# Performance work log

Measured on AMD Instinct MI355X. Metric: run time of the kernel, lower is better.

Reference implementation:

```python
import jax, jax.numpy as jnp
import numpy as np

N_NODES = 50000
N_EDGES = 400000
N_FEAT = 128
HIDDEN = 128
N_HEADS = 4
HEADC = HIDDEN // N_HEADS  # 32
N_CLASSES = 10
K_HOPS = 3
CST = 1e-5


def setup_inputs() -> dict:
    key = jax.random.key(0)
    ks = jax.random.split(key, 12)
    s = 1.0 / np.sqrt(HIDDEN)
    return {
        "node_feat": jax.random.normal(ks[0], (N_NODES, N_FEAT), jnp.float32),
        "edge_index": jax.random.randint(ks[1], (2, N_EDGES), 0, N_NODES, jnp.int64),
        # Linear weights stored as [in, out] so forward is x @ W + b
        "Wt": jax.random.normal(ks[2], (N_FEAT, HIDDEN), jnp.float32) / np.sqrt(N_FEAT),
        "bt": jax.random.normal(ks[3], (HIDDEN,), jnp.float32) * 0.01,
        "Wq": jax.random.normal(ks[4], (HIDDEN, N_HEADS * HEADC), jnp.float32) * s,
        "bq": jax.random.normal(ks[5], (N_HEADS * HEADC,), jnp.float32) * 0.01,
        "Wk": jax.random.normal(ks[6], (HIDDEN, N_HEADS * HEADC), jnp.float32) * s,
        "bk": jax.random.normal(ks[7], (N_HEADS * HEADC,), jnp.float32) * 0.01,
        "Wv": jax.random.normal(ks[8], (HIDDEN, N_HEADS * N_CLASSES), jnp.float32) * s,
        "bv": jax.random.normal(ks[9], (N_HEADS * N_CLASSES,), jnp.float32) * 0.01,
        "hopwise": jnp.ones((K_HOPS + 1,), jnp.float32),          # Parameter(ones(K+1))
        "headwise": jax.random.normal(ks[10], (N_HEADS, K_HOPS), jnp.float32) * 0.1,  # Parameter, zeros at init; randomized for testing
    }


def reference(node_feat, edge_index, Wt, bt, Wq, bq, Wk, bk, Wv, bv, hopwise, headwise):
    N = node_feat.shape[0]
    row, col = edge_index[0], edge_index[1]

    # eval mode: dropout is identity
    x = jax.nn.relu(node_feat @ Wt + bt)                       # [N, hidden]
    Q = (1.0 + jax.nn.elu(x @ Wq + bq)).reshape(N, N_HEADS, HEADC)
    Kf = (1.0 + jax.nn.elu(x @ Wk + bk)).reshape(N, N_HEADS, HEADC)
    V = (x @ Wv + bv).reshape(N, N_HEADS, N_CLASSES)

    M = jnp.einsum('nhi,nhj->nhij', Kf, V)                     # [N, H, headc, C]
    hidden = V * hopwise[0]                                     # ind_gamma & gamma_softmax branch
    layerwise = jax.nn.softmax(headwise, axis=0)                # softmax over heads (dim=-2)

    for hop in range(K_HOPS):
        # PyG sum aggregation, source_to_target: out[col] += x[row]
        M = jax.ops.segment_sum(M[row], col, num_segments=N)
        Kf = jax.ops.segment_sum(Kf[row], col, num_segments=N)
        H = jnp.einsum('nhi,nhij->nhj', Q, M)                  # [N, H, C]
        C = jnp.einsum('nhi,nhi->nh', Q, Kf)[..., None] + CST  # [N, H, 1]
        H = H / C
        gamma = hopwise[hop + 1] * layerwise[:, hop][:, None]  # [H, 1]
        hidden = hidden + gamma * H

    return hidden.sum(axis=-2)                                  # multi_concat=False: sum over heads -> [N, C]
```

## Files before the change

kernel.cpp:

```cpp
#include <hip/hip_runtime.h>
#include <hip/hip_bf16.h>

#define NN 50000
#define NE 400000
#define NF 128
#define HID 128
#define NH 4
#define HC 32
#define NC 10
#define KHOPS 3
#define NBLK ((NN + 1023) / 1024)

typedef unsigned int uint;
typedef unsigned short ushort;
typedef __attribute__((ext_vector_type(8))) short bf16x8;
typedef __attribute__((ext_vector_type(4))) float f32x4;
typedef __attribute__((ext_vector_type(2))) float f32x2;

__global__ void detect_kernel(const int* __restrict__ ei, int* __restrict__ flag) {
    int w = ei[2 * threadIdx.x + 1];
    unsigned long long b = __ballot(w != 0);
    if (threadIdx.x == 0) *flag = (b == 0ULL) ? 1 : 0;
}

__device__ __forceinline__ int edge_row(const int* ei, int is64, int e) {
    return is64 ? ei[2 * e] : ei[e];
}
__device__ __forceinline__ int edge_col(const int* ei, int is64, int e) {
    return is64 ? ei[2 * NE + 2 * e] : ei[NE + e];
}

__global__ void zero_kernel(int* __restrict__ p, int n) {
    int i = blockIdx.x * blockDim.x + threadIdx.x;
    if (i < n) p[i] = 0;
}

__global__ void hist_kernel(const int* __restrict__ ei, const int* __restrict__ flag,
                            int* __restrict__ counts) {
    int e = blockIdx.x * blockDim.x + threadIdx.x;
    if (e >= NE) return;
    int c = edge_col(ei, *flag, e);
    atomicAdd(&counts[c], 1);
}

__global__ __launch_bounds__(256) void bsum_kernel(const int* __restrict__ counts,
                                                   int* __restrict__ bsum) {
    int b = blockIdx.x, tid = threadIdx.x;
    int base = b * 1024 + tid * 4;
    int4 v = {0, 0, 0, 0};
    if (base < NN) v = *(const int4*)(counts + base);
    int s = v.x + v.y + v.z + v.w;
#pragma unroll
    for (int off = 32; off >= 1; off >>= 1) s += __shfl_xor(s, off);
    __shared__ int ws[4];
    int lane = tid & 63, w = tid >> 6;
    if (lane == 0) ws[w] = s;
    __syncthreads();
    if (tid == 0) bsum[b] = ws[0] + ws[1] + ws[2] + ws[3];
}

__global__ void bscan_kernel(const int* __restrict__ bsum, int* __restrict__ boff,
                             int* __restrict__ rowptr) {
    int lane = threadIdx.x;
    int v = (lane < NBLK) ? bsum[lane] : 0;
    int t = v;
#pragma unroll
    for (int off = 1; off < 64; off <<= 1) {
        int u = __shfl_up(t, off);
        if (lane >= off) t += u;
    }
    if (lane < NBLK) boff[lane] = t - v;
    if (lane == NBLK - 1) rowptr[NN] = t;
}

__global__ __launch_bounds__(256) void scanb_kernel(const int* __restrict__ counts,
                                                    const int* __restrict__ boff,
                                                    int* __restrict__ rowptr,
                                                    int* __restrict__ cursor) {
    int b = blockIdx.x, tid = threadIdx.x;
    int base = b * 1024 + tid * 4;
    int4 v = {0, 0, 0, 0};
    if (base < NN) v = *(const int4*)(counts + base);
    int s3 = v.x + v.y + v.z + v.w;
    int lane = tid & 63, w = tid >> 6;
    int t = s3;
#pragma unroll
    for (int off = 1; off < 64; off <<= 1) {
        int u = __shfl_up(t, off);
        if (lane >= off) t += u;
    }
    __shared__ int ws[4];
    if (lane == 63) ws[w] = t;
    __syncthreads();
    int wofs = boff[b];
    for (int i = 0; i < 4; i++) wofs += (i < w) ? ws[i] : 0;
    int excl = wofs + t - s3;
    if (base < NN) {
        int4 o;
        o.x = excl;
        o.y = excl + v.x;
        o.z = o.y + v.y;
        o.w = o.z + v.z;
        *(int4*)(rowptr + base) = o;
        *(int4*)(cursor + base) = o;
    }
}

__global__ void scatter_kernel(const int* __restrict__ ei, const int* __restrict__ flag,
                               int* __restrict__ cursor, int* __restrict__ srows) {
    int e = blockIdx.x * blockDim.x + threadIdx.x;
    if (e >= NE) return;
    int is64 = *flag;
    int r = edge_row(ei, is64, e);
    int c = edge_col(ei, is64, e);
    int pos = atomicAdd(&cursor[c], 1);
    srows[pos] = r;
}

__device__ __forceinline__ short bfbits(float f) {
    __hip_bfloat16 h = __float2bfloat16(f);
    return *reinterpret_cast<short*>(&h);
}
__device__ __forceinline__ ushort bfbitsu(float f) {
    __hip_bfloat16 h = __float2bfloat16(f);
    return *reinterpret_cast<ushort*>(&h);
}
__device__ __forceinline__ float bflo(uint u) { return __uint_as_float(u << 16); }
__device__ __forceinline__ float bfhi(uint u) { return __uint_as_float(u & 0xFFFF0000u); }
__device__ __forceinline__ float bfs(ushort u) { return __uint_as_float(((uint)u) << 16); }

template<bool HI>
__device__ __forceinline__ uint pk8(float a, float b, uint old) {
    return __builtin_amdgcn_cvt_pk_fp8_f32(a, b, old, HI);
}
template<bool HI>
__device__ __forceinline__ f32x2 upk8(uint w) {
    return __builtin_amdgcn_cvt_pk_f32_fp8(w, HI);
}

__global__ void wconv_kernel(const float* __restrict__ Wt, const float* __restrict__ Wq,
                             const float* __restrict__ Wk, const float* __restrict__ Wv,
                             ushort* __restrict__ Wtb, ushort* __restrict__ Wqkvb) {
    int idx = blockIdx.x * 256 + threadIdx.x;
    if (idx < 128 * 128) {
        int c = idx >> 7, k = idx & 127;
        Wtb[c * 128 + k] = bfbitsu(Wt[k * 128 + c]);
    }
    if (idx < 304 * 128) {
        int c = idx >> 7, k = idx & 127;
        float w;
        if (c < 128) w = Wq[k * 128 + c];
        else if (c < 256) w = Wk[k * 128 + (c - 128)];
        else { int cv = c - 256; w = (cv < 40) ? Wv[k * 40 + cv] : 0.f; }
        Wqkvb[c * 128 + k] = bfbitsu(w);
    }
}

__global__ __launch_bounds__(256) void xm_kernel(const float* __restrict__ nf,
                                                 const ushort* __restrict__ Wtb,
                                                 const float* __restrict__ bt,
                                                 ushort* __restrict__ xb) {
    int wid = threadIdx.x >> 6, lane = threadIdx.x & 63;
    int row0 = blockIdx.x * 64 + wid * 16;
    int r = lane & 15, kg = lane >> 4;
    int ar = row0 + r;
    if (ar > NN - 1) ar = NN - 1;
    int ctbeg = blockIdx.y * 4;
    f32x4 acc[4];
#pragma unroll
    for (int ct = 0; ct < 4; ct++) acc[ct] = f32x4{0.f, 0.f, 0.f, 0.f};
#pragma unroll
    for (int ks = 0; ks < 4; ks++) {
        int k0 = ks * 32 + kg * 8;
        const float4* ap = (const float4*)(nf + (size_t)ar * 128 + k0);
        float4 a0 = ap[0], a1 = ap[1];
        bf16x8 af;
        af[0] = bfbits(a0.x); af[1] = bfbits(a0.y); af[2] = bfbits(a0.z); af[3] = bfbits(a0.w);
        af[4] = bfbits(a1.x); af[5] = bfbits(a1.y); af[6] = bfbits(a1.z); af[7] = bfbits(a1.w);
#pragma unroll
        for (int ct = 0; ct < 4; ct++) {
            bf16x8 bfr = *(const bf16x8*)(Wtb + (size_t)((ctbeg + ct) * 16 + r) * 128 + k0);
            acc[ct] = __builtin_amdgcn_mfma_f32_16x16x32_bf16(af, bfr, acc[ct], 0, 0, 0);
        }
    }
#pragma unroll
    for (int ct = 0; ct < 4; ct++) {
        int c = (ctbeg + ct) * 16 + r;
        float b = bt[c];
#pragma unroll
        for (int reg = 0; reg < 4; reg++) {
            int n = row0 + kg * 4 + reg;
            if (n < NN) {
                float z = acc[ct][reg] + b;
                xb[(size_t)n * 128 + c] = bfbitsu(fmaxf(z, 0.f));
            }
        }
    }
}

template<int CTBEG, int NCT>
__device__ __forceinline__ void qkv_body(const ushort* __restrict__ xb,
                                         const ushort* __restrict__ Wqkvb,
                                         const float* __restrict__ bq,
                                         const float* __restrict__ bk,
                                         const float* __restrict__ bv,
                                         float* __restrict__ Qp,
                                         ushort* __restrict__ Kpp,
                                         ushort* __restrict__ Vbf,
                                         int row0, int r, int kg) {
    int ar = row0 + r;
    if (ar > NN - 1) ar = NN - 1;
    f32x4 acc[NCT];
#pragma unroll
    for (int ct = 0; ct < NCT; ct++) acc[ct] = f32x4{0.f, 0.f, 0.f, 0.f};
#pragma unroll
    for (int ks = 0; ks < 4; ks++) {
        int k0 = ks * 32 + kg * 8;
        bf16x8 af = *(const bf16x8*)(xb + (size_t)ar * 128 + k0);
#pragma unroll
        for (int ct = 0; ct < NCT; ct++) {
            bf16x8 bfr = *(const bf16x8*)(Wqkvb + (size_t)((CTBEG + ct) * 16 + r) * 128 + k0);
            acc[ct] = __builtin_amdgcn_mfma_f32_16x16x32_bf16(af, bfr, acc[ct], 0, 0, 0);
        }
    }
#pragma unroll
    for (int ct = 0; ct < NCT; ct++) {
        int c = (CTBEG + ct) * 16 + r;
        float bias;
        if (c < 128) bias = bq[c];
        else if (c < 256) bias = bk[c - 128];
        else { int cv = c - 256; bias = (cv < 40) ? bv[cv] : 0.f; }
#pragma unroll
        for (int reg = 0; reg < 4; reg++) {
            int n = row0 + kg * 4 + reg;
            if (n >= NN) continue;
            float z = acc[ct][reg] + bias;
            if (c < 128) {
                float q = z > 0.f ? 1.f + z : __expf(z);
                Qp[(size_t)n * 128 + c] = q;
            } else if (c < 256) {
                int cc = c - 128;
                float kv = z > 0.f ? 1.f + z : __expf(z);
                Kpp[(size_t)n * 128 + cc] = bfbitsu(kv);
            } else {
                int cv = c - 256;
                if (cv < 40) {
                    int hh = cv / 10, cc = cv - hh * 10;
                    Vbf[(size_t)n * 64 + hh * 16 + cc] = bfbitsu(z);
                }
            }
        }
    }
}

__global__ __launch_bounds__(256) void qkv_kernel(const ushort* __restrict__ xb,
                                                  const ushort* __restrict__ Wqkvb,
                                                  const float* __restrict__ bq,
                                                  const float* __restrict__ bk,
                                                  const float* __restrict__ bv,
                                                  float* __restrict__ Qp,
                                                  ushort* __restrict__ Kpp,
                                                  ushort* __restrict__ Vbf) {
    int wid = threadIdx.x >> 6, lane = threadIdx.x & 63;
    int row0 = blockIdx.x * 64 + wid * 16;
    int r = lane & 15, kg = lane >> 4;
    if (blockIdx.y == 0)
        qkv_body<0, 8>(xb, Wqkvb, bq, bk, bv, Qp, Kpp, Vbf, row0, r, kg);
    else if (blockIdx.y == 1)
        qkv_body<8, 8>(xb, Wqkvb, bq, bk, bv, Qp, Kpp, Vbf, row0, r, kg);
    else
        qkv_body<16, 3>(xb, Wqkvb, bq, bk, bv, Qp, Kpp, Vbf, row0, r, kg);
}

__global__ void vinit_kernel(float* __restrict__ out, const ushort* __restrict__ Vbf,
                             const float* __restrict__ hopwise) {
    int idx = blockIdx.x * blockDim.x + threadIdx.x;
    if (idx >= NN * NC) return;
    int n = idx / NC, c = idx - n * NC;
    const ushort* v = Vbf + (size_t)n * 64 + c;
    out[idx] = hopwise[0] * (bfs(v[0]) + bfs(v[16]) + bfs(v[32]) + bfs(v[48]));
}

__device__ __forceinline__ void fused_epilog(float a0[10], float a1[10], float k0a, float k1a,
                                             int gw, int lane,
                                             const float* __restrict__ Qp,
                                             float* __restrict__ out,
                                             uint4* __restrict__ Mq4n, uint* __restrict__ Mrun,
                                             ushort* __restrict__ Kn,
                                             const float* __restrict__ hopwise,
                                             const float* __restrict__ headwise,
                                             int hop, int write_next,
                                             float h_scale, float ss) {
    int p0 = lane * 2;
    float2 q = *(const float2*)(Qp + (size_t)gw * 128 + p0);
    float num[10];
#pragma unroll
    for (int c = 0; c < 10; c++) num[c] = q.x * a0[c] + q.y * a1[c];
    float den = q.x * k0a + q.y * k1a;
#pragma unroll
    for (int off = 8; off >= 1; off >>= 1) {
#pragma unroll
        for (int c = 0; c < 10; c++) num[c] += __shfl_xor(num[c], off);
        den += __shfl_xor(den, off);
    }
    float e0 = __expf(headwise[0 * KHOPS + hop]);
    float e1 = __expf(headwise[1 * KHOPS + hop]);
    float e2 = __expf(headwise[2 * KHOPS + hop]);
    float e3 = __expf(headwise[3 * KHOPS + hop]);
    int h = lane >> 4;
    float eh = (h == 0) ? e0 : (h == 1) ? e1 : (h == 2) ? e2 : e3;
    float gamma = hopwise[hop + 1] * eh / (e0 + e1 + e2 + e3);
    float s = h_scale * gamma / (den + 1e-5f);
    float tot[10];
#pragma unroll
    for (int c = 0; c < 10; c++) {
        tot[c] = s * num[c];
        tot[c] += __shfl_xor(tot[c], 16);
        tot[c] += __shfl_xor(tot[c], 32);
    }
    if (lane < 10) {
        float v = lane == 0 ? tot[0] : lane == 1 ? tot[1] : lane == 2 ? tot[2] :
                  lane == 3 ? tot[3] : lane == 4 ? tot[4] : lane == 5 ? tot[5] :
                  lane == 6 ? tot[6] : lane == 7 ? tot[7] : lane == 8 ? tot[8] : tot[9];
        out[(size_t)gw * 10 + lane] += v;
    }
    if (write_next) {
        uint4 o;
        uint x = pk8<false>(a0[0] * ss, a0[1] * ss, 0u);
        o.x = pk8<true>(a0[2] * ss, a0[3] * ss, x);
        x = pk8<false>(a0[4] * ss, a0[5] * ss, 0u);
        o.y = pk8<true>(a0[6] * ss, a0[7] * ss, x);
        x = pk8<false>(a1[0] * ss, a1[1] * ss, 0u);
        o.z = pk8<true>(a1[2] * ss, a1[3] * ss, x);
        x = pk8<false>(a1[4] * ss, a1[5] * ss, 0u);
        o.w = pk8<true>(a1[6] * ss, a1[7] * ss, x);
        Mq4n[(size_t)gw * 64 + lane] = o;
        x = pk8<false>(a0[8] * ss, a0[9] * ss, 0u);
        x = pk8<true>(a1[8] * ss, a1[9] * ss, x);
        Mrun[(size_t)gw * 64 + lane] = x;
        uint kw = (uint)bfbitsu(k0a) | (((uint)bfbitsu(k1a)) << 16);
        *(uint*)(Kn + (size_t)gw * 128 + p0) = kw;
    }
}

__device__ __forceinline__ void edge_acc(float a0[10], float a1[10], float& k0a, float& k1a,
                                         uint4 mq, uint mr, uint kk) {
    f32x2 f;
    f = upk8<false>(mq.x); a0[0] += f.x; a0[1] += f.y;
    f = upk8<true>(mq.x);  a0[2] += f.x; a0[3] += f.y;
    f = upk8<false>(mq.y); a0[4] += f.x; a0[5] += f.y;
    f = upk8<true>(mq.y);  a0[6] += f.x; a0[7] += f.y;
    f = upk8<false>(mq.z); a1[0] += f.x; a1[1] += f.y;
    f = upk8<true>(mq.z);  a1[2] += f.x; a1[3] += f.y;
    f = upk8<false>(mq.w); a1[4] += f.x; a1[5] += f.y;
    f = upk8<true>(mq.w);  a1[6] += f.x; a1[7] += f.y;
    f = upk8<false>(mr);   a0[8] += f.x; a0[9] += f.y;
    f = upk8<true>(mr);    a1[8] += f.x; a1[9] += f.y;
    k0a += bflo(kk);
    k1a += bfhi(kk);
}

__global__ __launch_bounds__(256) void aggf0_kernel(const ushort* __restrict__ Kpp,
                                                    const ushort* __restrict__ Vbf,
                                                    const float* __restrict__ Qp,
                                                    float* __restrict__ out,
                                                    uint4* __restrict__ Mq4n, uint* __restrict__ Mrun,
                                                    ushort* __restrict__ Kn,
                                                    const int* __restrict__ rowptr,
                                                    const int* __restrict__ srows,
                                                    const float* __restrict__ hopwise,
                                                    const float* __restrict__ headwise) {
    int gw = (blockIdx.x * 256 + threadIdx.x) >> 6;
    int lane = threadIdx.x & 63;
    int p0 = lane * 2;
    int h = lane >> 4;
    int beg = rowptr[gw], end = rowptr[gw + 1];
    float a0[10] = {0.f}, a1[10] = {0.f};
    float k0a = 0.f, k1a = 0.f;
    int e = beg;
    for (; e + 1 < end; e += 2) {
        int s0 = srows[e], s1 = srows[e + 1];
        uint kk0 = *(const uint*)(Kpp + (size_t)s0 * 128 + p0);
        uint kk1 = *(const uint*)(Kpp + (size_t)s1 * 128 + p0);
        const ushort* vb0 = Vbf + (size_t)s0 * 64 + h * 16;
        const ushort* vb1 = Vbf + (size_t)s1 * 64 + h * 16;
        uint4 v40 = *(const uint4*)vb0; uint v10 = *(const uint*)(vb0 + 8);
        uint4 v41 = *(const uint4*)vb1; uint v11 = *(const uint*)(vb1 + 8);
        float k00 = bflo(kk0), k01 = bfhi(kk0);
        float k10 = bflo(kk1), k11 = bfhi(kk1);
        k0a += k00 + k10; k1a += k01 + k11;
        float vv0[10] = {bflo(v40.x), bfhi(v40.x), bflo(v40.y), bfhi(v40.y), bflo(v40.z),
                         bfhi(v40.z), bflo(v40.w), bfhi(v40.w), bflo(v10), bfhi(v10)};
        float vv1[10] = {bflo(v41.x), bfhi(v41.x), bflo(v41.y), bfhi(v41.y), bflo(v41.z),
                         bfhi(v41.z), bflo(v41.w), bfhi(v41.w), bflo(v11), bfhi(v11)};
#pragma unroll
        for (int c = 0; c < 10; c++) {
            a0[c] += k00 * vv0[c] + k10 * vv1[c];
            a1[c] += k01 * vv0[c] + k11 * vv1[c];
        }
    }
    for (; e < end; ++e) {
        int s0 = srows[e];
        uint kk0 = *(const uint*)(Kpp + (size_t)s0 * 128 + p0);
        const ushort* vb0 = Vbf + (size_t)s0 * 64 + h * 16;
        uint4 v40 = *(const uint4*)vb0; uint v10 = *(const uint*)(vb0 + 8);
        float k00 = bflo(kk0), k01 = bfhi(kk0);
        k0a += k00; k1a += k01;
        float vv0[10] = {bflo(v40.x), bfhi(v40.x), bflo(v40.y), bfhi(v40.y), bflo(v40.z),
                         bfhi(v40.z), bflo(v40.w), bfhi(v40.w), bflo(v10), bfhi(v10)};
#pragma unroll
        for (int c = 0; c < 10; c++) {
            a0[c] += k00 * vv0[c];
            a1[c] += k01 * vv0[c];
        }
    }
    fused_epilog(a0, a1, k0a, k1a, gw, lane, Qp, out, Mq4n, Mrun, Kn,
                 hopwise, headwise, 0, 1, 1.0f, 0.0625f);
}

__global__ __launch_bounds__(256) void aggf_kernel(const uint4* __restrict__ Mq4,
                                                   const uint* __restrict__ Mru,
                                                   const ushort* __restrict__ Kc,
                                                   const float* __restrict__ Qp,
                                                   float* __restrict__ out,
                                                   uint4* __restrict__ Mq4n, uint* __restrict__ Mrun,
                                                   ushort* __restrict__ Kn,
                                                   const int* __restrict__ rowptr,
                                                   const int* __restrict__ srows,
                                                   const float* __restrict__ hopwise,
                                                   const float* __restrict__ headwise,
                                                   int hop, int write_next) {
    int gw = (blockIdx.x * 256 + threadIdx.x) >> 6;
    int lane = threadIdx.x & 63;
    const uint* Kcu = (const uint*)Kc;
    int beg = rowptr[gw], end = rowptr[gw + 1];
    float a0[10] = {0.f}, a1[10] = {0.f};
    float k0a = 0.f, k1a = 0.f;
    int e = beg;
    for (; e + 3 < end; e += 4) {
        int s0 = srows[e], s1 = srows[e + 1], s2 = srows[e + 2], s3 = srows[e + 3];
        uint4 m0 = Mq4[(size_t)s0 * 64 + lane];
        uint4 m1 = Mq4[(size_t)s1 * 64 + lane];
        uint4 m2 = Mq4[(size_t)s2 * 64 + lane];
        uint4 m3 = Mq4[(size_t)s3 * 64 + lane];
        uint r0 = Mru[(size_t)s0 * 64 + lane];
        uint r1 = Mru[(size_t)s1 * 64 + lane];
        uint r2 = Mru[(size_t)s2 * 64 + lane];
        uint r3 = Mru[(size_t)s3 * 64 + lane];
        uint K0 = Kcu[(size_t)s0 * 64 + lane];
        uint K1 = Kcu[(size_t)s1 * 64 + lane];
        uint K2 = Kcu[(size_t)s2 * 64 + lane];
        uint K3 = Kcu[(size_t)s3 * 64 + lane];
        edge_acc(a0, a1, k0a, k1a, m0, r0, K0);
        edge_acc(a0, a1, k0a, k1a, m1, r1, K1);
        edge_acc(a0, a1, k0a, k1a, m2, r2, K2);
        edge_acc(a0, a1, k0a, k1a, m3, r3, K3);
    }
    for (; e < end; ++e) {
        int s0 = srows[e];
        uint4 m0 = Mq4[(size_t)s0 * 64 + lane];
        uint r0 = Mru[(size_t)s0 * 64 + lane];
        uint K0 = Kcu[(size_t)s0 * 64 + lane];
        edge_acc(a0, a1, k0a, k1a, m0, r0, K0);
    }
    fused_epilog(a0, a1, k0a, k1a, gw, lane, Qp, out, Mq4n, Mrun, Kn,
                 hopwise, headwise, hop, write_next, 16.0f, 1.0f);
}

extern "C" void kernel_launch(void* const* d_in, const int* in_sizes, int n_in,
                              void* d_out, int out_size, void* d_ws, size_t ws_size,
                              hipStream_t stream) {
    const float* nf = (const float*)d_in[0];
    const int* ei = (const int*)d_in[1];
    const float* Wt = (const float*)d_in[2];
    const float* bt = (const float*)d_in[3];
    const float* Wq = (const float*)d_in[4];
    const float* bq = (const float*)d_in[5];
    const float* Wk = (const float*)d_in[6];
    const float* bk = (const float*)d_in[7];
    const float* Wv = (const float*)d_in[8];
    const float* bv = (const float*)d_in[9];
    const float* hopwise = (const float*)d_in[10];
    const float* headwise = (const float*)d_in[11];
    float* out = (float*)d_out;

    char* p = (char*)d_ws;
    auto alloc = [&](size_t bytes) {
        char* r = p;
        p += (bytes + 255) & ~(size_t)255;
        return r;
    };
    int* rowptr = (int*)alloc((NN + 4) * sizeof(int));
    int* cursor = (int*)alloc((NN + 4) * sizeof(int));
    int* bsum = (int*)alloc(NBLK * sizeof(int));
    int* boff = (int*)alloc(NBLK * sizeof(int));
    int* srows = (int*)alloc((size_t)NE * sizeof(int));
    int* flag = (int*)alloc(sizeof(int));
    ushort* Wtb = (ushort*)alloc(128 * 128 * sizeof(ushort));
    ushort* Wqkvb = (ushort*)alloc(304 * 128 * sizeof(ushort));
    float* Qp = (float*)alloc((size_t)NN * 128 * sizeof(float));
    ushort* Kpp = (ushort*)alloc((size_t)NN * 128 * sizeof(ushort));
    ushort* Vbf = (ushort*)alloc((size_t)NN * 64 * sizeof(ushort));
    ushort* Ka = (ushort*)alloc((size_t)NN * 128 * sizeof(ushort));
    uint4* Mq4a = (uint4*)alloc((size_t)NN * 64 * sizeof(uint4));
    uint4* Mq4b = (uint4*)alloc((size_t)NN * 64 * sizeof(uint4));
    uint* Mrua = (uint*)alloc((size_t)NN * 64 * sizeof(uint));
    uint* Mrub = (uint*)alloc((size_t)NN * 64 * sizeof(uint));
    ushort* xb = (ushort*)Mq4a;
    ushort* Kb = Kpp;

    detect_kernel<<<1, 64, 0, stream>>>(ei, flag);
    zero_kernel<<<(NN + 255) / 256, 256, 0, stream>>>(cursor, NN);
    hist_kernel<<<(NE + 255) / 256, 256, 0, stream>>>(ei, flag, cursor);
    bsum_kernel<<<NBLK, 256, 0, stream>>>(cursor, bsum);
    bscan_kernel<<<1, 64, 0, stream>>>(bsum, boff, rowptr);
    scanb_kernel<<<NBLK, 256, 0, stream>>>(cursor, boff, rowptr, cursor);
    scatter_kernel<<<(NE + 255) / 256, 256, 0, stream>>>(ei, flag, cursor, srows);

    wconv_kernel<<<(304 * 128 + 255) / 256, 256, 0, stream>>>(Wt, Wq, Wk, Wv, Wtb, Wqkvb);
    int nrb = (NN + 63) / 64;
    xm_kernel<<<dim3(nrb, 2), 256, 0, stream>>>(nf, Wtb, bt, xb);
    qkv_kernel<<<dim3(nrb, 3), 256, 0, stream>>>(xb, Wqkvb, bq, bk, bv, Qp, Kpp, Vbf);
    vinit_kernel<<<(NN * NC + 255) / 256, 256, 0, stream>>>(out, Vbf, hopwise);

    aggf0_kernel<<<NN / 4, 256, 0, stream>>>(Kpp, Vbf, Qp, out, Mq4a, Mrua, Ka,
                                             rowptr, srows, hopwise, headwise);
    aggf_kernel<<<NN / 4, 256, 0, stream>>>(Mq4a, Mrua, Ka, Qp, out, Mq4b, Mrub, Kb,
                                            rowptr, srows, hopwise, headwise, 1, 1);
    aggf_kernel<<<NN / 4, 256, 0, stream>>>(Mq4b, Mrub, Kb, Qp, out, Mq4a, Mrua, Ka,
                                            rowptr, srows, hopwise, headwise, 2, 0);
}
```

Baseline: 391.1 us.

## Store K features in fp8 with 1/16 scale and use packed f32x2 accumulation

```diff
diff --git a/kernel.cpp b/kernel.cpp
--- a/kernel.cpp
+++ b/kernel.cpp
@@ -128,6 +128,9 @@
 __device__ __forceinline__ float bflo(uint u) { return __uint_as_float(u << 16); }
 __device__ __forceinline__ float bfhi(uint u) { return __uint_as_float(u & 0xFFFF0000u); }
 __device__ __forceinline__ float bfs(ushort u) { return __uint_as_float(((uint)u) << 16); }
+__device__ __forceinline__ f32x2 bf2(uint u) {
+    return f32x2{__uint_as_float(u << 16), __uint_as_float(u & 0xFFFF0000u)};
+}
 
 template<bool HI>
 __device__ __forceinline__ uint pk8(float a, float b, uint old) {
@@ -205,7 +208,7 @@
                                          const float* __restrict__ bk,
                                          const float* __restrict__ bv,
                                          float* __restrict__ Qp,
-                                         ushort* __restrict__ Kpp,
+                                         unsigned char* __restrict__ K8,
                                          ushort* __restrict__ Vbf,
                                          int row0, int r, int kg) {
     int ar = row0 + r;
@@ -240,8 +243,9 @@
                 Qp[(size_t)n * 128 + c] = q;
             } else if (c < 256) {
                 int cc = c - 128;
-                float kv = z > 0.f ? 1.f + z : __expf(z);
-                Kpp[(size_t)n * 128 + cc] = bfbitsu(kv);
+                float kv = (z > 0.f ? 1.f + z : __expf(z)) * 0.0625f;
+                uint w = pk8<false>(kv, 0.f, 0u);
+                K8[(size_t)n * 128 + cc] = (unsigned char)(w & 0xFF);
             } else {
                 int cv = c - 256;
                 if (cv < 40) {
@@ -259,17 +263,17 @@
                                                   const float* __restrict__ bk,
                                                   const float* __restrict__ bv,
                                                   float* __restrict__ Qp,
-                                                  ushort* __restrict__ Kpp,
+                                                  unsigned char* __restrict__ K8,
                                                   ushort* __restrict__ Vbf) {
     int wid = threadIdx.x >> 6, lane = threadIdx.x & 63;
     int row0 = blockIdx.x * 64 + wid * 16;
     int r = lane & 15, kg = lane >> 4;
     if (blockIdx.y == 0)
-        qkv_body<0, 8>(xb, Wqkvb, bq, bk, bv, Qp, Kpp, Vbf, row0, r, kg);
+        qkv_body<0, 8>(xb, Wqkvb, bq, bk, bv, Qp, K8, Vbf, row0, r, kg);
     else if (blockIdx.y == 1)
-        qkv_body<8, 8>(xb, Wqkvb, bq, bk, bv, Qp, Kpp, Vbf, row0, r, kg);
+        qkv_body<8, 8>(xb, Wqkvb, bq, bk, bv, Qp, K8, Vbf, row0, r, kg);
     else
-        qkv_body<16, 3>(xb, Wqkvb, bq, bk, bv, Qp, Kpp, Vbf, row0, r, kg);
+        qkv_body<16, 3>(xb, Wqkvb, bq, bk, bv, Qp, K8, Vbf, row0, r, kg);
 }
 
 __global__ void vinit_kernel(float* __restrict__ out, const ushort* __restrict__ Vbf,
@@ -281,22 +285,24 @@
     out[idx] = hopwise[0] * (bfs(v[0]) + bfs(v[16]) + bfs(v[32]) + bfs(v[48]));
 }
 
-__device__ __forceinline__ void fused_epilog(float a0[10], float a1[10], float k0a, float k1a,
+__device__ __forceinline__ void fused_epilog(f32x2 A0[5], f32x2 A1[5], f32x2 kA,
                                              int gw, int lane,
                                              const float* __restrict__ Qp,
                                              float* __restrict__ out,
                                              uint4* __restrict__ Mq4n, uint* __restrict__ Mrun,
-                                             ushort* __restrict__ Kn,
+                                             ushort* __restrict__ K8n,
                                              const float* __restrict__ hopwise,
                                              const float* __restrict__ headwise,
-                                             int hop, int write_next,
-                                             float h_scale, float ss) {
+                                             int hop, int write_next) {
     int p0 = lane * 2;
     float2 q = *(const float2*)(Qp + (size_t)gw * 128 + p0);
     float num[10];
 #pragma unroll
-    for (int c = 0; c < 10; c++) num[c] = q.x * a0[c] + q.y * a1[c];
-    float den = q.x * k0a + q.y * k1a;
+    for (int j = 0; j < 5; j++) {
+        num[2 * j] = q.x * A0[j].x + q.y * A1[j].x;
+        num[2 * j + 1] = q.x * A0[j].y + q.y * A1[j].y;
+    }
+    float den = q.x * kA.x + q.y * kA.y;
 #pragma unroll
     for (int off = 8; off >= 1; off >>= 1) {
 #pragma unroll
@@ -310,7 +316,7 @@
     int h = lane >> 4;
     float eh = (h == 0) ? e0 : (h == 1) ? e1 : (h == 2) ? e2 : e3;
     float gamma = hopwise[hop + 1] * eh / (e0 + e1 + e2 + e3);
-    float s = h_scale * gamma / (den + 1e-5f);
+    float s = gamma / (den + 6.25e-7f);
     float tot[10];
 #pragma unroll
     for (int c = 0; c < 10; c++) {
@@ -326,105 +332,98 @@
     }
     if (write_next) {
         uint4 o;
-        uint x = pk8<false>(a0[0] * ss, a0[1] * ss, 0u);
-        o.x = pk8<true>(a0[2] * ss, a0[3] * ss, x);
-        x = pk8<false>(a0[4] * ss, a0[5] * ss, 0u);
-        o.y = pk8<true>(a0[6] * ss, a0[7] * ss, x);
-        x = pk8<false>(a1[0] * ss, a1[1] * ss, 0u);
-        o.z = pk8<true>(a1[2] * ss, a1[3] * ss, x);
-        x = pk8<false>(a1[4] * ss, a1[5] * ss, 0u);
-        o.w = pk8<true>(a1[6] * ss, a1[7] * ss, x);
+        o.x = pk8<true>(A0[1].x, A0[1].y, pk8<false>(A0[0].x, A0[0].y, 0u));
+        o.y = pk8<true>(A0[3].x, A0[3].y, pk8<false>(A0[2].x, A0[2].y, 0u));
+        o.z = pk8<true>(A1[1].x, A1[1].y, pk8<false>(A1[0].x, A1[0].y, 0u));
+        o.w = pk8<true>(A1[3].x, A1[3].y, pk8<false>(A1[2].x, A1[2].y, 0u));
         Mq4n[(size_t)gw * 64 + lane] = o;
-        x = pk8<false>(a0[8] * ss, a0[9] * ss, 0u);
-        x = pk8<true>(a1[8] * ss, a1[9] * ss, x);
-        Mrun[(size_t)gw * 64 + lane] = x;
-        uint kw = (uint)bfbitsu(k0a) | (((uint)bfbitsu(k1a)) << 16);
-        *(uint*)(Kn + (size_t)gw * 128 + p0) = kw;
-    }
-}
-
-__device__ __forceinline__ void edge_acc(float a0[10], float a1[10], float& k0a, float& k1a,
+        Mrun[(size_t)gw * 64 + lane] =
+            pk8<true>(A1[4].x, A1[4].y, pk8<false>(A0[4].x, A0[4].y, 0u));
+        uint kw = pk8<false>(kA.x, kA.y, 0u);
+        K8n[(size_t)gw * 64 + lane] = (ushort)(kw & 0xFFFF);
+    }
+}
+
+__device__ __forceinline__ void edge_acc(f32x2 A0[5], f32x2 A1[5], f32x2& kA,
                                          uint4 mq, uint mr, uint kk) {
-    f32x2 f;
-    f = upk8<false>(mq.x); a0[0] += f.x; a0[1] += f.y;
-    f = upk8<true>(mq.x);  a0[2] += f.x; a0[3] += f.y;
-    f = upk8<false>(mq.y); a0[4] += f.x; a0[5] += f.y;
-    f = upk8<true>(mq.y);  a0[6] += f.x; a0[7] += f.y;
-    f = upk8<false>(mq.z); a1[0] += f.x; a1[1] += f.y;
-    f = upk8<true>(mq.z);  a1[2] += f.x; a1[3] += f.y;
-    f = upk8<false>(mq.w); a1[4] += f.x; a1[5] += f.y;
-    f = upk8<true>(mq.w);  a1[6] += f.x; a1[7] += f.y;
-    f = upk8<false>(mr);   a0[8] += f.x; a0[9] += f.y;
-    f = upk8<true>(mr);    a1[8] += f.x; a1[9] += f.y;
-    k0a += bflo(kk);
-    k1a += bfhi(kk);
-}
-
-__global__ __launch_bounds__(256) void aggf0_kernel(const ushort* __restrict__ Kpp,
+    A0[0] += upk8<false>(mq.x);
+    A0[1] += upk8<true>(mq.x);
+    A0[2] += upk8<false>(mq.y);
+    A0[3] += upk8<true>(mq.y);
+    A1[0] += upk8<false>(mq.z);
+    A1[1] += upk8<true>(mq.z);
+    A1[2] += upk8<false>(mq.w);
+    A1[3] += upk8<true>(mq.w);
+    A0[4] += upk8<false>(mr);
+    A1[4] += upk8<true>(mr);
+    kA += upk8<false>(kk);
+}
+
+__global__ __launch_bounds__(256) void aggf0_kernel(const ushort* __restrict__ K8c,
                                                     const ushort* __restrict__ Vbf,
                                                     const float* __restrict__ Qp,
                                                     float* __restrict__ out,
                                                     uint4* __restrict__ Mq4n, uint* __restrict__ Mrun,
-                                                    ushort* __restrict__ Kn,
+                                                    ushort* __restrict__ K8n,
                                                     const int* __restrict__ rowptr,
                                                     const int* __restrict__ srows,
                                                     const float* __restrict__ hopwise,
                                                     const float* __restrict__ headwise) {
     int gw = (blockIdx.x * 256 + threadIdx.x) >> 6;
     int lane = threadIdx.x & 63;
-    int p0 = lane * 2;
     int h = lane >> 4;
     int beg = rowptr[gw], end = rowptr[gw + 1];
-    float a0[10] = {0.f}, a1[10] = {0.f};
-    float k0a = 0.f, k1a = 0.f;
+    f32x2 A0[5], A1[5], kA = f32x2{0.f, 0.f};
+#pragma unroll
+    for (int j = 0; j < 5; j++) { A0[j] = f32x2{0.f, 0.f}; A1[j] = f32x2{0.f, 0.f}; }
     int e = beg;
     for (; e + 1 < end; e += 2) {
         int s0 = srows[e], s1 = srows[e + 1];
-        uint kk0 = *(const uint*)(Kpp + (size_t)s0 * 128 + p0);
-        uint kk1 = *(const uint*)(Kpp + (size_t)s1 * 128 + p0);
+        uint k0w = K8c[(size_t)s0 * 64 + lane];
+        uint k1w = K8c[(size_t)s1 * 64 + lane];
         const ushort* vb0 = Vbf + (size_t)s0 * 64 + h * 16;
         const ushort* vb1 = Vbf + (size_t)s1 * 64 + h * 16;
         uint4 v40 = *(const uint4*)vb0; uint v10 = *(const uint*)(vb0 + 8);
         uint4 v41 = *(const uint4*)vb1; uint v11 = *(const uint*)(vb1 + 8);
-        float k00 = bflo(kk0), k01 = bfhi(kk0);
-        float k10 = bflo(kk1), k11 = bfhi(kk1);
-        k0a += k00 + k10; k1a += k01 + k11;
-        float vv0[10] = {bflo(v40.x), bfhi(v40.x), bflo(v40.y), bfhi(v40.y), bflo(v40.z),
-                         bfhi(v40.z), bflo(v40.w), bfhi(v40.w), bflo(v10), bfhi(v10)};
-        float vv1[10] = {bflo(v41.x), bfhi(v41.x), bflo(v41.y), bfhi(v41.y), bflo(v41.z),
-                         bfhi(v41.z), bflo(v41.w), bfhi(v41.w), bflo(v11), bfhi(v11)};
-#pragma unroll
-        for (int c = 0; c < 10; c++) {
-            a0[c] += k00 * vv0[c] + k10 * vv1[c];
-            a1[c] += k01 * vv0[c] + k11 * vv1[c];
+        f32x2 kk0 = upk8<false>(k0w);
+        f32x2 kk1 = upk8<false>(k1w);
+        kA += kk0 + kk1;
+        f32x2 V0[5] = {bf2(v40.x), bf2(v40.y), bf2(v40.z), bf2(v40.w), bf2(v10)};
+        f32x2 V1[5] = {bf2(v41.x), bf2(v41.y), bf2(v41.z), bf2(v41.w), bf2(v11)};
+        f32x2 k00 = f32x2{kk0.x, kk0.x}, k01 = f32x2{kk0.y, kk0.y};
+        f32x2 k10 = f32x2{kk1.x, kk1.x}, k11 = f32x2{kk1.y, kk1.y};
+#pragma unroll
+        for (int j = 0; j < 5; j++) {
+            A0[j] += k00 * V0[j] + k10 * V1[j];
+            A1[j] += k01 * V0[j] + k11 * V1[j];
         }
     }
     for (; e < end; ++e) {
         int s0 = srows[e];
-        uint kk0 = *(const uint*)(Kpp + (size_t)s0 * 128 + p0);
+        uint k0w = K8c[(size_t)s0 * 64 + lane];
         const ushort* vb0 = Vbf + (size_t)s0 * 64 + h * 16;
         uint4 v40 = *(const uint4*)vb0; uint v10 = *(const uint*)(vb0 + 8);
-        float k00 = bflo(kk0), k01 = bfhi(kk0);
-        k0a += k00; k1a += k01;
-        float vv0[10] = {bflo(v40.x), bfhi(v40.x), bflo(v40.y), bfhi(v40.y), bflo(v40.z),
-                         bfhi(v40.z), bflo(v40.w), bfhi(v40.w), bflo(v10), bfhi(v10)};
-#pragma unroll
-        for (int c = 0; c < 10; c++) {
-            a0[c] += k00 * vv0[c];
-            a1[c] += k01 * vv0[c];
+        f32x2 kk0 = upk8<false>(k0w);
+        kA += kk0;
+        f32x2 V0[5] = {bf2(v40.x), bf2(v40.y), bf2(v40.z), bf2(v40.w), bf2(v10)};
+        f32x2 k00 = f32x2{kk0.x, kk0.x}, k01 = f32x2{kk0.y, kk0.y};
+#pragma unroll
+        for (int j = 0; j < 5; j++) {
+            A0[j] += k00 * V0[j];
+            A1[j] += k01 * V0[j];
         }
     }
-    fused_epilog(a0, a1, k0a, k1a, gw, lane, Qp, out, Mq4n, Mrun, Kn,
-                 hopwise, headwise, 0, 1, 1.0f, 0.0625f);
+    fused_epilog(A0, A1, kA, gw, lane, Qp, out, Mq4n, Mrun, K8n,
+                 hopwise, headwise, 0, 1);
 }
 
 __global__ __launch_bounds__(256) void aggf_kernel(const uint4* __restrict__ Mq4,
                                                    const uint* __restrict__ Mru,
-                                                   const ushort* __restrict__ Kc,
+                                                   const ushort* __restrict__ K8c,
                                                    const float* __restrict__ Qp,
                                                    float* __restrict__ out,
                                                    uint4* __restrict__ Mq4n, uint* __restrict__ Mrun,
-                                                   ushort* __restrict__ Kn,
+                                                   ushort* __restrict__ K8n,
                                                    const int* __restrict__ rowptr,
                                                    const int* __restrict__ srows,
                                                    const float* __restrict__ hopwise,
@@ -432,39 +431,48 @@
                                                    int hop, int write_next) {
     int gw = (blockIdx.x * 256 + threadIdx.x) >> 6;
     int lane = threadIdx.x & 63;
-    const uint* Kcu = (const uint*)Kc;
     int beg = rowptr[gw], end = rowptr[gw + 1];
-    float a0[10] = {0.f}, a1[10] = {0.f};
-    float k0a = 0.f, k1a = 0.f;
+    f32x2 A0[5], A1[5], kA = f32x2{0.f, 0.f};
+#pragma unroll
+    for (int j = 0; j < 5; j++) { A0[j] = f32x2{0.f, 0.f}; A1[j] = f32x2{0.f, 0.f}; }
     int e = beg;
-    for (; e + 3 < end; e += 4) {
-        int s0 = srows[e], s1 = srows[e + 1], s2 = srows[e + 2], s3 = srows[e + 3];
+    for (; e + 5 < end; e += 6) {
+        int s0 = srows[e], s1 = srows[e + 1], s2 = srows[e + 2];
+        int s3 = srows[e + 3], s4 = srows[e + 4], s5 = srows[e + 5];
         uint4 m0 = Mq4[(size_t)s0 * 64 + lane];
         uint4 m1 = Mq4[(size_t)s1 * 64 + lane];
         uint4 m2 = Mq4[(size_t)s2 * 64 + lane];
         uint4 m3 = Mq4[(size_t)s3 * 64 + lane];
+        uint4 m4 = Mq4[(size_t)s4 * 64 + lane];
+        uint4 m5 = Mq4[(size_t)s5 * 64 + lane];
         uint r0 = Mru[(size_t)s0 * 64 + lane];
         uint r1 = Mru[(size_t)s1 * 64 + lane];
         uint r2 = Mru[(size_t)s2 * 64 + lane];
         uint r3 = Mru[(size_t)s3 * 64 + lane];
-        uint K0 = Kcu[(size_t)s0 * 64 + lane];
-        uint K1 = Kcu[(size_t)s1 * 64 + lane];
-        uint K2 = Kcu[(size_t)s2 * 64 + lane];
-        uint K3 = Kcu[(size_t)s3 * 64 + lane];
-        edge_acc(a0, a1, k0a, k1a, m0, r0, K0);
-        edge_acc(a0, a1, k0a, k1a, m1, r1, K1);
-        edge_acc(a0, a1, k0a, k1a, m2, r2, K2);
-        edge_acc(a0, a1, k0a, k1a, m3, r3, K3);
+        uint r4 = Mru[(size_t)s4 * 64 + lane];
+        uint r5 = Mru[(size_t)s5 * 64 + lane];
+        uint k0 = K8c[(size_t)s0 * 64 + lane];
+        uint k1 = K8c[(size_t)s1 * 64 + lane];
+        uint k2 = K8c[(size_t)s2 * 64 + lane];
+        uint k3 = K8c[(size_t)s3 * 64 + lane];
+        uint k4 = K8c[(size_t)s4 * 64 + lane];
+        uint k5 = K8c[(size_t)s5 * 64 + lane];
+        edge_acc(A0, A1, kA, m0, r0, k0);
+        edge_acc(A0, A1, kA, m1, r1, k1);
+        edge_acc(A0, A1, kA, m2, r2, k2);
+        edge_acc(A0, A1, kA, m3, r3, k3);
+        edge_acc(A0, A1, kA, m4, r4, k4);
+        edge_acc(A0, A1, kA, m5, r5, k5);
     }
     for (; e < end; ++e) {
         int s0 = srows[e];
         uint4 m0 = Mq4[(size_t)s0 * 64 + lane];
         uint r0 = Mru[(size_t)s0 * 64 + lane];
-        uint K0 = Kcu[(size_t)s0 * 64 + lane];
-        edge_acc(a0, a1, k0a, k1a, m0, r0, K0);
-    }
-    fused_epilog(a0, a1, k0a, k1a, gw, lane, Qp, out, Mq4n, Mrun, Kn,
-                 hopwise, headwise, hop, write_next, 16.0f, 1.0f);
+        uint k0 = K8c[(size_t)s0 * 64 + lane];
+        edge_acc(A0, A1, kA, m0, r0, k0);
+    }
+    fused_epilog(A0, A1, kA, gw, lane, Qp, out, Mq4n, Mrun, K8n,
+                 hopwise, headwise, hop, write_next);
 }
 
 extern "C" void kernel_launch(void* const* d_in, const int* in_sizes, int n_in,
@@ -499,15 +507,15 @@
     ushort* Wtb = (ushort*)alloc(128 * 128 * sizeof(ushort));
     ushort* Wqkvb = (ushort*)alloc(304 * 128 * sizeof(ushort));
     float* Qp = (float*)alloc((size_t)NN * 128 * sizeof(float));
-    ushort* Kpp = (ushort*)alloc((size_t)NN * 128 * sizeof(ushort));
+    unsigned char* K8pp = (unsigned char*)alloc((size_t)NN * 128);
     ushort* Vbf = (ushort*)alloc((size_t)NN * 64 * sizeof(ushort));
-    ushort* Ka = (ushort*)alloc((size_t)NN * 128 * sizeof(ushort));
+    ushort* K8a = (ushort*)alloc((size_t)NN * 64 * sizeof(ushort));
     uint4* Mq4a = (uint4*)alloc((size_t)NN * 64 * sizeof(uint4));
     uint4* Mq4b = (uint4*)alloc((size_t)NN * 64 * sizeof(uint4));
     uint* Mrua = (uint*)alloc((size_t)NN * 64 * sizeof(uint));
     uint* Mrub = (uint*)alloc((size_t)NN * 64 * sizeof(uint));
     ushort* xb = (ushort*)Mq4a;
-    ushort* Kb = Kpp;
+    ushort* K8b = (ushort*)K8pp;
 
     detect_kernel<<<1, 64, 0, stream>>>(ei, flag);
     zero_kernel<<<(NN + 255) / 256, 256, 0, stream>>>(cursor, NN);
@@ -520,13 +528,14 @@
     wconv_kernel<<<(304 * 128 + 255) / 256, 256, 0, stream>>>(Wt, Wq, Wk, Wv, Wtb, Wqkvb);
     int nrb = (NN + 63) / 64;
     xm_kernel<<<dim3(nrb, 2), 256, 0, stream>>>(nf, Wtb, bt, xb);
-    qkv_kernel<<<dim3(nrb, 3), 256, 0, stream>>>(xb, Wqkvb, bq, bk, bv, Qp, Kpp, Vbf);
+    qkv_kernel<<<dim3(nrb, 3), 256, 0, stream>>>(xb, Wqkvb, bq, bk, bv, Qp, K8pp, Vbf);
     vinit_kernel<<<(NN * NC + 255) / 256, 256, 0, stream>>>(out, Vbf, hopwise);
 
-    aggf0_kernel<<<NN / 4, 256, 0, stream>>>(Kpp, Vbf, Qp, out, Mq4a, Mrua, Ka,
+    aggf0_kernel<<<NN / 4, 256, 0, stream>>>((const ushort*)K8pp, Vbf, Qp, out,
+                                             Mq4a, Mrua, K8a,
                                              rowptr, srows, hopwise, headwise);
-    aggf_kernel<<<NN / 4, 256, 0, stream>>>(Mq4a, Mrua, Ka, Qp, out, Mq4b, Mrub, Kb,
+    aggf_kernel<<<NN / 4, 256, 0, stream>>>(Mq4a, Mrua, K8a, Qp, out, Mq4b, Mrub, K8b,
                                             rowptr, srows, hopwise, headwise, 1, 1);
-    aggf_kernel<<<NN / 4, 256, 0, stream>>>(Mq4b, Mrub, Kb, Qp, out, Mq4a, Mrua, Ka,
+    aggf_kernel<<<NN / 4, 256, 0, stream>>>(Mq4b, Mrub, K8b, Qp, out, Mq4a, Mrua, K8a,
                                             rowptr, srows, hopwise, headwise, 2, 0);
 }
```

Result: slower. 410.3 us (+4.9%).
